# Kernel tuning notes

Hardware: AMD Instinct MI355X
Metric: run time of the kernel (lower is better)

The kernel has to match this reference:

```python
import jax, jax.numpy as jnp
import numpy as np

H = 8          # n_heads
THRESH = 0.5   # edge pruning threshold
LN_EPS = 1e-5


def setup_inputs() -> dict:
    key = jax.random.key(0)
    ks = jax.random.split(key, 24)
    B, S, D = 8, 128, 256
    N = S + 1
    hd = D // H

    def lin(k, fan_in, fan_out, gain=1.0):
        # xavier_uniform-ish init, stored as [in, out] (y = x @ W + b)
        lim = gain * np.sqrt(6.0 / (fan_in + fan_out))
        return jax.random.uniform(k, (fan_in, fan_out), jnp.float32, -lim, lim)

    g = 1.0 / np.sqrt(2.0)
    return {
        "desc": jax.random.normal(ks[0], (B, S, D), jnp.float32),
        "nv": jax.random.normal(ks[1], (B, N, D), jnp.float32),
        "W_gt": lin(ks[2], D, D), "b_gt": jnp.zeros((D,), jnp.float32),
        "topo_bias": jnp.zeros((1,), jnp.float32),
        "W_q": lin(ks[3], D, D, g), "b_q": jnp.zeros((D,), jnp.float32),
        "W_k": lin(ks[4], D, D, g), "b_k": jnp.zeros((D,), jnp.float32),
        "W_v": lin(ks[5], D, D, g), "b_v": jnp.zeros((D,), jnp.float32),
        "W_e1": lin(ks[6], 2 * D, D), "b_e1": jnp.zeros((D,), jnp.float32),
        "ln_g": jnp.ones((D,), jnp.float32), "ln_b": jnp.zeros((D,), jnp.float32),
        "W_e2": lin(ks[7], D, D), "b_e2": jnp.zeros((D,), jnp.float32),
        "w_attn": lin(ks[8], 3 * hd, 1, g)[:, 0], "b_attn": jnp.zeros((), jnp.float32),
        "W_o": lin(ks[9], D, D, g), "b_o": jnp.zeros((D,), jnp.float32),
    }


def _forward(desc, nv, W_gt, b_gt, topo_bias, W_q, b_q, W_k, b_k, W_v, b_v,
             W_e1, b_e1, ln_g, ln_b, W_e2, b_e2, w_attn, b_attn, W_o, b_o):
    B, N, D = nv.shape
    S = N - 1
    hd = D // H

    # 1. global topology
    d = desc @ W_gt + b_gt                                   # [B,S,D]
    dn = d / jnp.linalg.norm(d, axis=-1, keepdims=True)
    global_top = jax.nn.sigmoid(jnp.einsum('bid,bjd->bij', dn, dn) + topo_bias[0])

    # 2. sample-wise similarity
    var = nv[:, 1:, :]
    vn = var / jnp.linalg.norm(var, axis=-1, keepdims=True)
    sample_sim = jnp.einsum('bid,bjd->bij', vn, vn)
    adj_mat = global_top * sample_sim

    # 3. remove self-connection, squash
    diag_mask = 1.0 - jnp.eye(S, dtype=adj_mat.dtype)
    adj = jax.nn.sigmoid(adj_mat * diag_mask)

    # 4. straight-through edge pruning (frozen=False path)
    hard = (adj > THRESH).astype(adj.dtype)
    adj = hard - jax.lax.stop_gradient(adj) + adj

    # 5. edge attributes: Linear(concat(d_i,d_j)) decomposed into two matmuls
    a = d @ W_e1[:D]                                          # node_i part [B,S,D]
    b_ = d @ W_e1[D:]                                         # node_j part [B,S,D]
    pre = jnp.zeros((B, N, N, D), dtype=d.dtype)
    pre = pre.at[:, 1:, 1:].set(a[:, :, None, :] + b_[:, None, :, :])
    cls = a + b_                                              # concat(d_j,d_j) rows
    pre = pre.at[:, 0, 1:].set(cls).at[:, 1:, 0].set(cls)
    pre = pre + b_e1                                          # (0,0) entry = bias only (zeros input)
    mu = pre.mean(-1, keepdims=True)
    vr = ((pre - mu) ** 2).mean(-1, keepdims=True)
    e = jax.nn.relu((pre - mu) * jax.lax.rsqrt(vr + LN_EPS) * ln_g + ln_b)
    e = e @ W_e2 + b_e2                                       # [B,N,N,D]
    e = e.reshape(B, N, N, H, hd).transpose(0, 3, 1, 2, 4)    # [B,H,N,N,hd]

    # padded adjacency: CLS row attends to all vars, col 0 masked
    na = jnp.zeros((B, N, N), dtype=adj.dtype)
    na = na.at[:, 1:, 1:].set(adj).at[:, 0, 1:].set(1.0)
    e = e * na[:, None, :, :, None]

    # 6. additive attention: attn_proj(concat(q,k,e)) decomposed
    q = (nv @ W_q + b_q).reshape(B, N, H, hd).transpose(0, 2, 1, 3)
    k = (nv @ W_k + b_k).reshape(B, N, H, hd).transpose(0, 2, 1, 3)
    v = (nv @ W_v + b_v).reshape(B, N, H, hd).transpose(0, 2, 1, 3)
    wq, wk, we = w_attn[:hd], w_attn[hd:2 * hd], w_attn[2 * hd:]
    scores = (jnp.einsum('bhid,d->bhi', q, wq)[:, :, :, None]
              + jnp.einsum('bhjd,d->bhj', k, wk)[:, :, None, :]
              + jnp.einsum('bhijd,d->bhij', e, we) + b_attn)
    scores = scores + (na[:, None, :, :] == 0).astype(scores.dtype) * -1e9
    attn = jax.nn.softmax(scores, axis=-1)                    # dropout = identity (eval)

    ctx = jnp.einsum('bhij,bhjd->bhid', attn, v)
    out = ctx.transpose(0, 2, 1, 3).reshape(B, N, D) @ W_o + b_o
    return out, attn


def reference(desc, nv, W_gt, b_gt, topo_bias, W_q, b_q, W_k, b_k, W_v, b_v,
              W_e1, b_e1, ln_g, ln_b, W_e2, b_e2, w_attn, b_attn, W_o, b_o):
    return _forward(desc, nv, W_gt, b_gt, topo_bias, W_q, b_q, W_k, b_k, W_v, b_v,
                    W_e1, b_e1, ln_g, ln_b, W_e2, b_e2, w_attn, b_attn, W_o, b_o)
```

## Files before the change

kernel.cpp:

```cpp
#include <hip/hip_runtime.h>
#include <math.h>

#define BB 8
#define SS 128
#define NN 129
#define DD 256
#define HH 8
#define LN_EPS 1e-5f

#define OFF_A    0
#define OFF_BPT  262144
#define OFF_CPT  524288
#define OFF_VART 786432
#define OFF_V    1048576
#define OFF_SQ   1312768
#define OFF_SK   1321024
#define OFF_MA   1329280
#define OFF_QA   1330304
#define OFF_MB   1331328
#define OFF_QB   1332352
#define OFF_MC   1333376
#define OFF_QC   1334400
#define OFF_U    1335424
#define OFF_UB   1337472

__global__ __launch_bounds__(256) void ka2(
    const float* __restrict__ desc, const float* __restrict__ nv,
    const float* __restrict__ W_gt, const float* __restrict__ b_gt,
    const float* __restrict__ W_e1, const float* __restrict__ b_e1,
    const float* __restrict__ W_q, const float* __restrict__ b_q,
    const float* __restrict__ W_k, const float* __restrict__ b_k,
    const float* __restrict__ W_v, const float* __restrict__ b_v,
    const float* __restrict__ W_e2, const float* __restrict__ b_e2,
    const float* __restrict__ w_attn,
    float* __restrict__ a, float* __restrict__ bp_t, float* __restrict__ cp_t,
    float* __restrict__ var_t, float* __restrict__ v,
    float* __restrict__ sq, float* __restrict__ sk,
    float* __restrict__ ma, float* __restrict__ qa, float* __restrict__ mb,
    float* __restrict__ qb, float* __restrict__ mc, float* __restrict__ qc,
    float* __restrict__ U, float* __restrict__ ubias) {
    const int bx = blockIdx.x, t = threadIdx.x;
    __shared__ __attribute__((aligned(16))) float rowbuf[DD][4];
    __shared__ __attribute__((aligned(16))) float drow[DD][4];
    __shared__ float part[24][4];

    if (bx < 256) {
        const int b = bx >> 5, s0 = (bx & 31) * 4;
        for (int e = t; e < 4 * DD; e += 256) {
            int r = e >> 8, k = e & 255;
            rowbuf[k][r] = desc[(size_t)(b * SS + s0 + r) * DD + k];
        }
        __syncthreads();
        const int c = t;
        {
            float dv[4] = {0.f, 0.f, 0.f, 0.f};
#pragma unroll 8
            for (int k = 0; k < DD; k++) {
                float w = W_gt[k * DD + c];
                float4 d4 = *(const float4*)&rowbuf[k][0];
                dv[0] = fmaf(d4.x, w, dv[0]); dv[1] = fmaf(d4.y, w, dv[1]);
                dv[2] = fmaf(d4.z, w, dv[2]); dv[3] = fmaf(d4.w, w, dv[3]);
            }
            float bg = b_gt[c];
            float4 st; st.x = dv[0] + bg; st.y = dv[1] + bg; st.z = dv[2] + bg; st.w = dv[3] + bg;
            *(float4*)&drow[c][0] = st;
        }
        __syncthreads();
        float av[4] = {0.f, 0.f, 0.f, 0.f}, bv[4] = {0.f, 0.f, 0.f, 0.f};
#pragma unroll 4
        for (int k = 0; k < DD; k++) {
            float wa = W_e1[k * DD + c];
            float wb = W_e1[(DD + k) * DD + c];
            float4 d4 = *(const float4*)&drow[k][0];
            av[0] = fmaf(d4.x, wa, av[0]); av[1] = fmaf(d4.y, wa, av[1]);
            av[2] = fmaf(d4.z, wa, av[2]); av[3] = fmaf(d4.w, wa, av[3]);
            bv[0] = fmaf(d4.x, wb, bv[0]); bv[1] = fmaf(d4.y, wb, bv[1]);
            bv[2] = fmaf(d4.z, wb, bv[2]); bv[3] = fmaf(d4.w, wb, bv[3]);
        }
        float be1 = b_e1[c];
        float cv[4];
#pragma unroll
        for (int r = 0; r < 4; r++) { bv[r] += be1; cv[r] = av[r] + bv[r]; }
#pragma unroll
        for (int r = 0; r < 4; r++) a[(size_t)(b * SS + s0 + r) * DD + c] = av[r];
        float4 f4;
        f4.x = bv[0]; f4.y = bv[1]; f4.z = bv[2]; f4.w = bv[3];
        *(float4*)(bp_t + (size_t)(b * DD + c) * SS + s0) = f4;
        f4.x = cv[0]; f4.y = cv[1]; f4.z = cv[2]; f4.w = cv[3];
        *(float4*)(cp_t + (size_t)(b * DD + c) * SS + s0) = f4;
        float nvv[4];
#pragma unroll
        for (int r = 0; r < 4; r++) nvv[r] = nv[(size_t)(b * NN + 1 + s0 + r) * DD + c];
        f4.x = nvv[0]; f4.y = nvv[1]; f4.z = nvv[2]; f4.w = nvv[3];
        *(float4*)(var_t + (size_t)(b * DD + c) * SS + s0) = f4;
        float vals[24];
#pragma unroll
        for (int r = 0; r < 4; r++) {
            vals[r * 6 + 0] = av[r]; vals[r * 6 + 1] = av[r] * av[r];
            vals[r * 6 + 2] = bv[r]; vals[r * 6 + 3] = bv[r] * bv[r];
            vals[r * 6 + 4] = cv[r]; vals[r * 6 + 5] = cv[r] * cv[r];
        }
        int lane = t & 63, wid = t >> 6;
#pragma unroll
        for (int vv = 0; vv < 24; vv++) {
            float x = vals[vv];
            for (int o = 32; o; o >>= 1) x += __shfl_xor(x, o, 64);
            if (lane == 0) part[vv][wid] = x;
        }
        __syncthreads();
        if (t < 24) {
            float ssum = (part[t][0] + part[t][1]) + (part[t][2] + part[t][3]);
            int st = t % 6;
            int row = b * SS + s0 + t / 6;
            float m = ssum * (1.f / DD);
            float* dstp = (st == 0) ? ma : (st == 1) ? qa : (st == 2) ? mb
                         : (st == 3) ? qb : (st == 4) ? mc : qc;
            dstp[row] = m;
        }
    } else if (bx < 520) {
        const int idx = bx - 256;
        const int b = idx / 33, n0 = (idx % 33) * 4;
        for (int e = t; e < 4 * DD; e += 256) {
            int r = e >> 8, k = e & 255;
            int n = n0 + r; if (n >= NN) n = NN - 1;
            rowbuf[k][r] = nv[(size_t)(b * NN + n) * DD + k];
        }
        __syncthreads();
        const int c = t;
        float qv[4] = {0.f, 0.f, 0.f, 0.f}, kv[4] = {0.f, 0.f, 0.f, 0.f},
              vv[4] = {0.f, 0.f, 0.f, 0.f};
#pragma unroll 4
        for (int k = 0; k < DD; k++) {
            float wq = W_q[k * DD + c], wk = W_k[k * DD + c], wvv = W_v[k * DD + c];
            float4 r4 = *(const float4*)&rowbuf[k][0];
            qv[0] = fmaf(r4.x, wq, qv[0]); qv[1] = fmaf(r4.y, wq, qv[1]);
            qv[2] = fmaf(r4.z, wq, qv[2]); qv[3] = fmaf(r4.w, wq, qv[3]);
            kv[0] = fmaf(r4.x, wk, kv[0]); kv[1] = fmaf(r4.y, wk, kv[1]);
            kv[2] = fmaf(r4.z, wk, kv[2]); kv[3] = fmaf(r4.w, wk, kv[3]);
            vv[0] = fmaf(r4.x, wvv, vv[0]); vv[1] = fmaf(r4.y, wvv, vv[1]);
            vv[2] = fmaf(r4.z, wvv, vv[2]); vv[3] = fmaf(r4.w, wvv, vv[3]);
        }
        float bq = b_q[c], bk = b_k[c], bvb = b_v[c];
        float waq = w_attn[c & 31];
        float wak = w_attn[32 + (c & 31)];
        int h = c >> 5;
#pragma unroll
        for (int r = 0; r < 4; r++) {
            int n = n0 + r;
            if (n < NN) v[(size_t)(b * NN + n) * DD + c] = vv[r] + bvb;
            float xq = (qv[r] + bq) * waq, xk = (kv[r] + bk) * wak;
#pragma unroll
            for (int o = 16; o; o >>= 1) { xq += __shfl_xor(xq, o); xk += __shfl_xor(xk, o); }
            if ((c & 31) == 0 && n < NN) {
                sq[(size_t)(b * HH + h) * NN + n] = xq;
                sk[(size_t)(b * HH + h) * NN + n] = xk;
            }
        }
    } else {
        const int ri = bx - 520;
        const int c = t;
        const float wec = w_attn[64 + (c & 31)];
#pragma unroll
        for (int rr = 0; rr < 4; rr++) {
            int r = ri * 4 + rr;
            float x = W_e2[(size_t)r * DD + c] * wec;
#pragma unroll
            for (int o = 16; o; o >>= 1) x += __shfl_xor(x, o);
            if ((c & 31) == 0) U[r * HH + (c >> 5)] = x;
        }
        if (ri == 0) {
            float x = b_e2[c] * wec;
#pragma unroll
            for (int o = 16; o; o >>= 1) x += __shfl_xor(x, o);
            if ((c & 31) == 0) ubias[c >> 5] = x;
        }
    }
}

__global__ __launch_bounds__(256) void kb2(
    const float* __restrict__ a, const float* __restrict__ bp_t, const float* __restrict__ cp_t,
    const float* __restrict__ var_t, const float* __restrict__ nv,
    const float* __restrict__ ma, const float* __restrict__ qa,
    const float* __restrict__ mb, const float* __restrict__ qb,
    const float* __restrict__ mc, const float* __restrict__ qc,
    const float* __restrict__ sq, const float* __restrict__ sk,
    const float* __restrict__ ln_g, const float* __restrict__ ln_b,
    const float* __restrict__ U, const float* __restrict__ ubias,
    const float* __restrict__ b_attn,
    float* __restrict__ attn) {
    const int i = blockIdx.x, b = blockIdx.y;
    const int t = threadIdx.x, jq = t & 31, dg = t >> 5;
    __shared__ float Arow[DD];
    __shared__ float Vrow[DD];
    __shared__ float2 lnsm[DD];
    __shared__ __attribute__((aligned(16))) float4 Usm[DD][2];
    __shared__ __attribute__((aligned(16))) float rsm[SS], nmm[SS], mkm[SS], pnm[SS];
    __shared__ float sqb[HH], ubm[HH];
    __shared__ float sc[HH][132];
    __shared__ __attribute__((aligned(16))) float red[8][HH * SS];

    Arow[t] = (i >= 1) ? a[((size_t)b * SS + i - 1) * DD + t] : 0.f;
    Vrow[t] = nv[((size_t)b * NN + i) * DD + t];
    { float2 g; g.x = ln_g[t]; g.y = ln_b[t]; lnsm[t] = g; }
    Usm[t][0] = *(const float4*)&U[t * HH];
    Usm[t][1] = *(const float4*)&U[t * HH + 4];
    if (t < HH) {
        sqb[t] = sq[(size_t)b * HH * NN + t * NN + i] + b_attn[0];
        ubm[t] = ubias[t];
    }
    __syncthreads();

    if (i >= 1) {
        float cr[4] = {0.f, 0.f, 0.f, 0.f}, dv[4] = {0.f, 0.f, 0.f, 0.f};
        const float* bc = bp_t + ((size_t)b * DD + dg * 32) * SS + 4 * jq;
        const float* vc = var_t + ((size_t)b * DD + dg * 32) * SS + 4 * jq;
#pragma unroll 8
        for (int dd = 0; dd < 32; dd++) {
            float4 b4 = *(const float4*)(bc + (size_t)dd * SS);
            float4 v4 = *(const float4*)(vc + (size_t)dd * SS);
            float A = Arow[dg * 32 + dd], V = Vrow[dg * 32 + dd];
            cr[0] = fmaf(A, b4.x, cr[0]); cr[1] = fmaf(A, b4.y, cr[1]);
            cr[2] = fmaf(A, b4.z, cr[2]); cr[3] = fmaf(A, b4.w, cr[3]);
            dv[0] = fmaf(V, v4.x, dv[0]); dv[1] = fmaf(V, v4.y, dv[1]);
            dv[2] = fmaf(V, v4.z, dv[2]); dv[3] = fmaf(V, v4.w, dv[3]);
        }
        float4 s0; s0.x = cr[0]; s0.y = cr[1]; s0.z = cr[2]; s0.w = cr[3];
        float4 s1; s1.x = dv[0]; s1.y = dv[1]; s1.z = dv[2]; s1.w = dv[3];
        *(float4*)&red[dg][4 * jq] = s0;
        *(float4*)&red[dg][SS + 4 * jq] = s1;
    }
    __syncthreads();
    if (t < SS) {
        const int j = t;
        float rs, nm, mk, pen;
        if (i == 0) {
            float mu = mc[b * SS + j], q2 = qc[b * SS + j];
            rs = rsqrtf(q2 - mu * mu + LN_EPS); nm = -mu * rs; mk = 1.f; pen = 0.f;
        } else {
            float cr = 0.f, dv = 0.f;
#pragma unroll
            for (int g = 0; g < 8; g++) { cr += red[g][j]; dv += red[g][SS + j]; }
            float muA = ma[b * SS + i - 1], qA = qa[b * SS + i - 1];
            float muB = mb[b * SS + j], qB = qb[b * SS + j];
            float mu = muA + muB;
            float var = qA + qB + 2.f * cr * (1.f / DD) - mu * mu;
            rs = rsqrtf(var + LN_EPS); nm = -mu * rs;
            mk = ((i - 1) != j && dv > 0.f) ? 1.f : 0.f;
            pen = (mk == 0.f) ? -1e9f : 0.f;
        }
        rsm[j] = rs; nmm[j] = nm; mkm[j] = mk; pnm[j] = pen;
    }
    __syncthreads();

    float acc[4][HH];
#pragma unroll
    for (int jj = 0; jj < 4; jj++)
#pragma unroll
        for (int h = 0; h < HH; h++) acc[jj][h] = 0.f;
    {
        const float* Bp = ((i == 0) ? cp_t : bp_t) + ((size_t)b * DD + dg * 32) * SS + 4 * jq;
        float4 rs4 = *(const float4*)&rsm[4 * jq];
        float4 nm4 = *(const float4*)&nmm[4 * jq];
        float rsv[4] = {rs4.x, rs4.y, rs4.z, rs4.w};
        float nmv[4] = {nm4.x, nm4.y, nm4.z, nm4.w};
#pragma unroll 4
        for (int dd = 0; dd < 32; dd++) {
            const int d2 = dg * 32 + dd;
            float4 b4 = *(const float4*)(Bp + (size_t)dd * SS);
            float A = Arow[d2];
            float2 gb = lnsm[d2];
            float4 u0 = Usm[d2][0], u1 = Usm[d2][1];
            float bj[4] = {b4.x, b4.y, b4.z, b4.w};
#pragma unroll
            for (int jj = 0; jj < 4; jj++) {
                float y = fmaf(A + bj[jj], rsv[jj], nmv[jj]);
                y = fmaf(y, gb.x, gb.y);
                float rr = fmaxf(y, 0.f);
                acc[jj][0] = fmaf(rr, u0.x, acc[jj][0]);
                acc[jj][1] = fmaf(rr, u0.y, acc[jj][1]);
                acc[jj][2] = fmaf(rr, u0.z, acc[jj][2]);
                acc[jj][3] = fmaf(rr, u0.w, acc[jj][3]);
                acc[jj][4] = fmaf(rr, u1.x, acc[jj][4]);
                acc[jj][5] = fmaf(rr, u1.y, acc[jj][5]);
                acc[jj][6] = fmaf(rr, u1.z, acc[jj][6]);
                acc[jj][7] = fmaf(rr, u1.w, acc[jj][7]);
            }
        }
    }
#pragma unroll
    for (int h = 0; h < HH; h++) {
        float4 w4;
        w4.x = acc[0][h]; w4.y = acc[1][h]; w4.z = acc[2][h]; w4.w = acc[3][h];
        *(float4*)&red[dg][h * SS + 4 * jq] = w4;
    }
    __syncthreads();
    {
        const int j = t >> 1, hb = (t & 1) * 4;
#pragma unroll
        for (int hh = 0; hh < 4; hh++) {
            int h = hb + hh;
            float s = 0.f;
#pragma unroll
            for (int g = 0; g < 8; g++) s += red[g][h * SS + j];
            float skv = sk[(size_t)b * HH * NN + h * NN + 1 + j];
            sc[h][1 + j] = sqb[h] + skv + (s + ubm[h]) * mkm[j] + pnm[j];
        }
    }
    if (t < HH) sc[t][0] = sqb[t] + sk[(size_t)b * HH * NN + t * NN] - 1e9f;
    __syncthreads();

    {
        const int h = t >> 5, l = t & 31;
        float m = -INFINITY;
        for (int jj = l; jj < NN; jj += 32) m = fmaxf(m, sc[h][jj]);
#pragma unroll
        for (int o = 16; o; o >>= 1) m = fmaxf(m, __shfl_xor(m, o));
        float s = 0.f;
        for (int jj = l; jj < NN; jj += 32) { float e = __expf(sc[h][jj] - m); sc[h][jj] = e; s += e; }
#pragma unroll
        for (int o = 16; o; o >>= 1) s += __shfl_xor(s, o);
        float inv = 1.f / s;
        float* arow = attn + (((size_t)b * HH + h) * NN + i) * NN;
        for (int jj = l; jj < NN; jj += 32) arow[jj] = sc[h][jj] * inv;
    }
}

__global__ __launch_bounds__(256) void kc2(
    const float* __restrict__ attn, const float* __restrict__ v,
    const float* __restrict__ W_o, const float* __restrict__ b_o,
    float* __restrict__ out) {
    const int b = blockIdx.y, i0 = blockIdx.x * 2;
    const int t = threadIdx.x;
    __shared__ float ar[2][HH * 132];
    __shared__ __attribute__((aligned(8))) float csm[DD][2];
    for (int e = t; e < 2 * HH * NN; e += 256) {
        int il = e / (HH * NN), r = e - il * (HH * NN);
        int h = r / NN, j = r - h * NN;
        int i = i0 + il; if (i >= NN) i = NN - 1;
        ar[il][h * 132 + j] = attn[(((size_t)b * HH + h) * NN + i) * NN + j];
    }
    __syncthreads();
    {
        const int d = t, h = d >> 5;
        float c0 = 0.f, c1 = 0.f;
        const float* vp = v + (size_t)b * NN * DD + d;
#pragma unroll 4
        for (int j = 0; j < NN; j++) {
            float vv = vp[(size_t)j * DD];
            c0 = fmaf(ar[0][h * 132 + j], vv, c0);
            c1 = fmaf(ar[1][h * 132 + j], vv, c1);
        }
        csm[d][0] = c0; csm[d][1] = c1;
    }
    __syncthreads();
    {
        const int c = t;
        float o0 = 0.f, o1 = 0.f;
#pragma unroll 8
        for (int k = 0; k < DD; k++) {
            float w = W_o[(size_t)k * DD + c];
            float2 cv = *(const float2*)&csm[k][0];
            o0 = fmaf(cv.x, w, o0); o1 = fmaf(cv.y, w, o1);
        }
        float bo = b_o[c];
        out[((size_t)b * NN + i0) * DD + c] = o0 + bo;
        if (i0 + 1 < NN) out[((size_t)b * NN + i0 + 1) * DD + c] = o1 + bo;
    }
}

extern "C" void kernel_launch(void* const* d_in, const int* in_sizes, int n_in,
                              void* d_out, int out_size, void* d_ws, size_t ws_size,
                              hipStream_t stream) {
    const float* desc   = (const float*)d_in[0];
    const float* nv     = (const float*)d_in[1];
    const float* W_gt   = (const float*)d_in[2];
    const float* b_gt   = (const float*)d_in[3];
    const float* W_q    = (const float*)d_in[5];
    const float* b_q    = (const float*)d_in[6];
    const float* W_k    = (const float*)d_in[7];
    const float* b_k    = (const float*)d_in[8];
    const float* W_v    = (const float*)d_in[9];
    const float* b_v    = (const float*)d_in[10];
    const float* W_e1   = (const float*)d_in[11];
    const float* b_e1   = (const float*)d_in[12];
    const float* ln_g   = (const float*)d_in[13];
    const float* ln_b   = (const float*)d_in[14];
    const float* W_e2   = (const float*)d_in[15];
    const float* b_e2   = (const float*)d_in[16];
    const float* w_attn = (const float*)d_in[17];
    const float* b_attn = (const float*)d_in[18];
    const float* W_o    = (const float*)d_in[19];
    const float* b_o    = (const float*)d_in[20];

    float* ws   = (float*)d_ws;
    float* a    = ws + OFF_A;
    float* bp_t = ws + OFF_BPT;
    float* cp_t = ws + OFF_CPT;
    float* vart = ws + OFF_VART;
    float* v    = ws + OFF_V;
    float* sq   = ws + OFF_SQ;
    float* sk   = ws + OFF_SK;
    float* ma   = ws + OFF_MA;
    float* qa   = ws + OFF_QA;
    float* mb   = ws + OFF_MB;
    float* qb   = ws + OFF_QB;
    float* mc   = ws + OFF_MC;
    float* qc   = ws + OFF_QC;
    float* U    = ws + OFF_U;
    float* ub   = ws + OFF_UB;

    float* out  = (float*)d_out;
    float* attn = (float*)d_out + (size_t)BB * NN * DD;

    ka2<<<dim3(584), dim3(256), 0, stream>>>(
        desc, nv, W_gt, b_gt, W_e1, b_e1, W_q, b_q, W_k, b_k, W_v, b_v,
        W_e2, b_e2, w_attn,
        a, bp_t, cp_t, vart, v, sq, sk, ma, qa, mb, qb, mc, qc, U, ub);
    kb2<<<dim3(NN, BB), dim3(256), 0, stream>>>(
        a, bp_t, cp_t, vart, nv, ma, qa, mb, qb, mc, qc, sq, sk,
        ln_g, ln_b, U, ub, b_attn, attn);
    kc2<<<dim3((NN + 1) / 2, BB), dim3(256), 0, stream>>>(attn, v, W_o, b_o, out);
}
```

Before: 191.2 us.

## Precompute Gram matrices in separate kernel and widen row tiles across kernels

```diff
diff --git a/kernel.cpp b/kernel.cpp
--- a/kernel.cpp
+++ b/kernel.cpp
@@ -23,8 +23,10 @@
 #define OFF_QC   1334400
 #define OFF_U    1335424
 #define OFF_UB   1337472
-
-__global__ __launch_bounds__(256) void ka2(
+#define OFF_G    1337600
+#define OFF_VV   1468672
+
+__global__ __launch_bounds__(256) void ka3(
     const float* __restrict__ desc, const float* __restrict__ nv,
     const float* __restrict__ W_gt, const float* __restrict__ b_gt,
     const float* __restrict__ W_e1, const float* __restrict__ b_e1,
@@ -40,75 +42,93 @@
     float* __restrict__ qb, float* __restrict__ mc, float* __restrict__ qc,
     float* __restrict__ U, float* __restrict__ ubias) {
     const int bx = blockIdx.x, t = threadIdx.x;
-    __shared__ __attribute__((aligned(16))) float rowbuf[DD][4];
-    __shared__ __attribute__((aligned(16))) float drow[DD][4];
-    __shared__ float part[24][4];
-
-    if (bx < 256) {
-        const int b = bx >> 5, s0 = (bx & 31) * 4;
-        for (int e = t; e < 4 * DD; e += 256) {
+    __shared__ __attribute__((aligned(16))) float rowbuf[DD][8];
+    __shared__ __attribute__((aligned(16))) float drow[DD][8];
+    __shared__ float part[48][4];
+
+    if (bx < 128) {
+        const int b = bx >> 4, s0 = (bx & 15) * 8;
+        for (int e = t; e < 8 * DD; e += 256) {
             int r = e >> 8, k = e & 255;
             rowbuf[k][r] = desc[(size_t)(b * SS + s0 + r) * DD + k];
         }
         __syncthreads();
         const int c = t;
         {
-            float dv[4] = {0.f, 0.f, 0.f, 0.f};
+            float dv[8] = {0.f, 0.f, 0.f, 0.f, 0.f, 0.f, 0.f, 0.f};
 #pragma unroll 8
             for (int k = 0; k < DD; k++) {
                 float w = W_gt[k * DD + c];
-                float4 d4 = *(const float4*)&rowbuf[k][0];
-                dv[0] = fmaf(d4.x, w, dv[0]); dv[1] = fmaf(d4.y, w, dv[1]);
-                dv[2] = fmaf(d4.z, w, dv[2]); dv[3] = fmaf(d4.w, w, dv[3]);
+                float4 d0 = *(const float4*)&rowbuf[k][0];
+                float4 d1 = *(const float4*)&rowbuf[k][4];
+                dv[0] = fmaf(d0.x, w, dv[0]); dv[1] = fmaf(d0.y, w, dv[1]);
+                dv[2] = fmaf(d0.z, w, dv[2]); dv[3] = fmaf(d0.w, w, dv[3]);
+                dv[4] = fmaf(d1.x, w, dv[4]); dv[5] = fmaf(d1.y, w, dv[5]);
+                dv[6] = fmaf(d1.z, w, dv[6]); dv[7] = fmaf(d1.w, w, dv[7]);
             }
             float bg = b_gt[c];
-            float4 st; st.x = dv[0] + bg; st.y = dv[1] + bg; st.z = dv[2] + bg; st.w = dv[3] + bg;
-            *(float4*)&drow[c][0] = st;
+            float4 s0v, s1v;
+            s0v.x = dv[0] + bg; s0v.y = dv[1] + bg; s0v.z = dv[2] + bg; s0v.w = dv[3] + bg;
+            s1v.x = dv[4] + bg; s1v.y = dv[5] + bg; s1v.z = dv[6] + bg; s1v.w = dv[7] + bg;
+            *(float4*)&drow[c][0] = s0v;
+            *(float4*)&drow[c][4] = s1v;
         }
         __syncthreads();
-        float av[4] = {0.f, 0.f, 0.f, 0.f}, bv[4] = {0.f, 0.f, 0.f, 0.f};
+        float av[8] = {0.f, 0.f, 0.f, 0.f, 0.f, 0.f, 0.f, 0.f};
+        float bv[8] = {0.f, 0.f, 0.f, 0.f, 0.f, 0.f, 0.f, 0.f};
 #pragma unroll 4
         for (int k = 0; k < DD; k++) {
             float wa = W_e1[k * DD + c];
             float wb = W_e1[(DD + k) * DD + c];
-            float4 d4 = *(const float4*)&drow[k][0];
-            av[0] = fmaf(d4.x, wa, av[0]); av[1] = fmaf(d4.y, wa, av[1]);
-            av[2] = fmaf(d4.z, wa, av[2]); av[3] = fmaf(d4.w, wa, av[3]);
-            bv[0] = fmaf(d4.x, wb, bv[0]); bv[1] = fmaf(d4.y, wb, bv[1]);
-            bv[2] = fmaf(d4.z, wb, bv[2]); bv[3] = fmaf(d4.w, wb, bv[3]);
+            float4 d0 = *(const float4*)&drow[k][0];
+            float4 d1 = *(const float4*)&drow[k][4];
+            av[0] = fmaf(d0.x, wa, av[0]); av[1] = fmaf(d0.y, wa, av[1]);
+            av[2] = fmaf(d0.z, wa, av[2]); av[3] = fmaf(d0.w, wa, av[3]);
+            av[4] = fmaf(d1.x, wa, av[4]); av[5] = fmaf(d1.y, wa, av[5]);
+            av[6] = fmaf(d1.z, wa, av[6]); av[7] = fmaf(d1.w, wa, av[7]);
+            bv[0] = fmaf(d0.x, wb, bv[0]); bv[1] = fmaf(d0.y, wb, bv[1]);
+            bv[2] = fmaf(d0.z, wb, bv[2]); bv[3] = fmaf(d0.w, wb, bv[3]);
+            bv[4] = fmaf(d1.x, wb, bv[4]); bv[5] = fmaf(d1.y, wb, bv[5]);
+            bv[6] = fmaf(d1.z, wb, bv[6]); bv[7] = fmaf(d1.w, wb, bv[7]);
         }
         float be1 = b_e1[c];
-        float cv[4];
-#pragma unroll
-        for (int r = 0; r < 4; r++) { bv[r] += be1; cv[r] = av[r] + bv[r]; }
-#pragma unroll
-        for (int r = 0; r < 4; r++) a[(size_t)(b * SS + s0 + r) * DD + c] = av[r];
+        float cv[8];
+#pragma unroll
+        for (int r = 0; r < 8; r++) { bv[r] += be1; cv[r] = av[r] + bv[r]; }
+#pragma unroll
+        for (int r = 0; r < 8; r++) a[(size_t)(b * SS + s0 + r) * DD + c] = av[r];
         float4 f4;
         f4.x = bv[0]; f4.y = bv[1]; f4.z = bv[2]; f4.w = bv[3];
         *(float4*)(bp_t + (size_t)(b * DD + c) * SS + s0) = f4;
+        f4.x = bv[4]; f4.y = bv[5]; f4.z = bv[6]; f4.w = bv[7];
+        *(float4*)(bp_t + (size_t)(b * DD + c) * SS + s0 + 4) = f4;
         f4.x = cv[0]; f4.y = cv[1]; f4.z = cv[2]; f4.w = cv[3];
         *(float4*)(cp_t + (size_t)(b * DD + c) * SS + s0) = f4;
-        float nvv[4];
-#pragma unroll
-        for (int r = 0; r < 4; r++) nvv[r] = nv[(size_t)(b * NN + 1 + s0 + r) * DD + c];
+        f4.x = cv[4]; f4.y = cv[5]; f4.z = cv[6]; f4.w = cv[7];
+        *(float4*)(cp_t + (size_t)(b * DD + c) * SS + s0 + 4) = f4;
+        float nvv[8];
+#pragma unroll
+        for (int r = 0; r < 8; r++) nvv[r] = nv[(size_t)(b * NN + 1 + s0 + r) * DD + c];
         f4.x = nvv[0]; f4.y = nvv[1]; f4.z = nvv[2]; f4.w = nvv[3];
         *(float4*)(var_t + (size_t)(b * DD + c) * SS + s0) = f4;
-        float vals[24];
-#pragma unroll
-        for (int r = 0; r < 4; r++) {
+        f4.x = nvv[4]; f4.y = nvv[5]; f4.z = nvv[6]; f4.w = nvv[7];
+        *(float4*)(var_t + (size_t)(b * DD + c) * SS + s0 + 4) = f4;
+        float vals[48];
+#pragma unroll
+        for (int r = 0; r < 8; r++) {
             vals[r * 6 + 0] = av[r]; vals[r * 6 + 1] = av[r] * av[r];
             vals[r * 6 + 2] = bv[r]; vals[r * 6 + 3] = bv[r] * bv[r];
             vals[r * 6 + 4] = cv[r]; vals[r * 6 + 5] = cv[r] * cv[r];
         }
         int lane = t & 63, wid = t >> 6;
 #pragma unroll
-        for (int vv = 0; vv < 24; vv++) {
+        for (int vv = 0; vv < 48; vv++) {
             float x = vals[vv];
             for (int o = 32; o; o >>= 1) x += __shfl_xor(x, o, 64);
             if (lane == 0) part[vv][wid] = x;
         }
         __syncthreads();
-        if (t < 24) {
+        if (t < 48) {
             float ssum = (part[t][0] + part[t][1]) + (part[t][2] + part[t][3]);
             int st = t % 6;
             int row = b * SS + s0 + t / 6;
@@ -117,35 +137,43 @@
                          : (st == 3) ? qb : (st == 4) ? mc : qc;
             dstp[row] = m;
         }
-    } else if (bx < 520) {
-        const int idx = bx - 256;
-        const int b = idx / 33, n0 = (idx % 33) * 4;
-        for (int e = t; e < 4 * DD; e += 256) {
+    } else if (bx < 264) {
+        const int idx = bx - 128;
+        const int b = idx / 17, n0 = (idx % 17) * 8;
+        for (int e = t; e < 8 * DD; e += 256) {
             int r = e >> 8, k = e & 255;
             int n = n0 + r; if (n >= NN) n = NN - 1;
             rowbuf[k][r] = nv[(size_t)(b * NN + n) * DD + k];
         }
         __syncthreads();
         const int c = t;
-        float qv[4] = {0.f, 0.f, 0.f, 0.f}, kv[4] = {0.f, 0.f, 0.f, 0.f},
-              vv[4] = {0.f, 0.f, 0.f, 0.f};
+        float qv[8] = {0.f, 0.f, 0.f, 0.f, 0.f, 0.f, 0.f, 0.f};
+        float kv[8] = {0.f, 0.f, 0.f, 0.f, 0.f, 0.f, 0.f, 0.f};
+        float vv[8] = {0.f, 0.f, 0.f, 0.f, 0.f, 0.f, 0.f, 0.f};
 #pragma unroll 4
         for (int k = 0; k < DD; k++) {
             float wq = W_q[k * DD + c], wk = W_k[k * DD + c], wvv = W_v[k * DD + c];
-            float4 r4 = *(const float4*)&rowbuf[k][0];
-            qv[0] = fmaf(r4.x, wq, qv[0]); qv[1] = fmaf(r4.y, wq, qv[1]);
-            qv[2] = fmaf(r4.z, wq, qv[2]); qv[3] = fmaf(r4.w, wq, qv[3]);
-            kv[0] = fmaf(r4.x, wk, kv[0]); kv[1] = fmaf(r4.y, wk, kv[1]);
-            kv[2] = fmaf(r4.z, wk, kv[2]); kv[3] = fmaf(r4.w, wk, kv[3]);
-            vv[0] = fmaf(r4.x, wvv, vv[0]); vv[1] = fmaf(r4.y, wvv, vv[1]);
-            vv[2] = fmaf(r4.z, wvv, vv[2]); vv[3] = fmaf(r4.w, wvv, vv[3]);
+            float4 r0 = *(const float4*)&rowbuf[k][0];
+            float4 r1 = *(const float4*)&rowbuf[k][4];
+            qv[0] = fmaf(r0.x, wq, qv[0]); qv[1] = fmaf(r0.y, wq, qv[1]);
+            qv[2] = fmaf(r0.z, wq, qv[2]); qv[3] = fmaf(r0.w, wq, qv[3]);
+            qv[4] = fmaf(r1.x, wq, qv[4]); qv[5] = fmaf(r1.y, wq, qv[5]);
+            qv[6] = fmaf(r1.z, wq, qv[6]); qv[7] = fmaf(r1.w, wq, qv[7]);
+            kv[0] = fmaf(r0.x, wk, kv[0]); kv[1] = fmaf(r0.y, wk, kv[1]);
+            kv[2] = fmaf(r0.z, wk, kv[2]); kv[3] = fmaf(r0.w, wk, kv[3]);
+            kv[4] = fmaf(r1.x, wk, kv[4]); kv[5] = fmaf(r1.y, wk, kv[5]);
+            kv[6] = fmaf(r1.z, wk, kv[6]); kv[7] = fmaf(r1.w, wk, kv[7]);
+            vv[0] = fmaf(r0.x, wvv, vv[0]); vv[1] = fmaf(r0.y, wvv, vv[1]);
+            vv[2] = fmaf(r0.z, wvv, vv[2]); vv[3] = fmaf(r0.w, wvv, vv[3]);
+            vv[4] = fmaf(r1.x, wvv, vv[4]); vv[5] = fmaf(r1.y, wvv, vv[5]);
+            vv[6] = fmaf(r1.z, wvv, vv[6]); vv[7] = fmaf(r1.w, wvv, vv[7]);
         }
         float bq = b_q[c], bk = b_k[c], bvb = b_v[c];
         float waq = w_attn[c & 31];
         float wak = w_attn[32 + (c & 31)];
         int h = c >> 5;
 #pragma unroll
-        for (int r = 0; r < 4; r++) {
+        for (int r = 0; r < 8; r++) {
             int n = n0 + r;
             if (n < NN) v[(size_t)(b * NN + n) * DD + c] = vv[r] + bvb;
             float xq = (qv[r] + bq) * waq, xk = (kv[r] + bk) * wak;
@@ -157,7 +185,7 @@
             }
         }
     } else {
-        const int ri = bx - 520;
+        const int ri = bx - 264;
         const int c = t;
         const float wec = w_attn[64 + (c & 31)];
 #pragma unroll
@@ -177,194 +205,240 @@
     }
 }
 
-__global__ __launch_bounds__(256) void kb2(
+__global__ __launch_bounds__(256) void kgram(
+    const float* __restrict__ a, const float* __restrict__ bp_t,
+    const float* __restrict__ nv, const float* __restrict__ var_t,
+    float* __restrict__ G, float* __restrict__ VV) {
+    const int bx = blockIdx.x, t = threadIdx.x;
+    const bool isG = bx < 128;
+    const int idx = isG ? bx : bx - 128;
+    const int b = idx >> 4, tl = idx & 15;
+    const int i0 = (tl >> 1) * 16, j0 = (tl & 1) * 64;
+    const float* Asrc = isG ? (a + ((size_t)b * SS + i0) * DD)
+                            : (nv + ((size_t)b * NN + 1 + i0) * DD);
+    const float* Bt = (isG ? bp_t : var_t) + (size_t)b * DD * SS;
+    float* C = (isG ? G : VV) + (size_t)b * SS * SS;
+    __shared__ __attribute__((aligned(16))) float Al[16][DD];
+    for (int e = t; e < 16 * DD / 4; e += 256) {
+        int r = e >> 6, c4 = e & 63;
+        *(float4*)&Al[r][c4 * 4] = *(const float4*)&Asrc[(size_t)r * DD + c4 * 4];
+    }
+    __syncthreads();
+    const int dg = t & 3, jl = t >> 2;
+    float acc[16] = {0.f, 0.f, 0.f, 0.f, 0.f, 0.f, 0.f, 0.f,
+                     0.f, 0.f, 0.f, 0.f, 0.f, 0.f, 0.f, 0.f};
+    const float* bp = Bt + (size_t)(dg * 64) * SS + j0 + jl;
+#pragma unroll 4
+    for (int dd = 0; dd < 64; dd++) {
+        float bvv = bp[(size_t)dd * SS];
+        int d = dg * 64 + dd;
+#pragma unroll
+        for (int i = 0; i < 16; i++) acc[i] = fmaf(Al[i][d], bvv, acc[i]);
+    }
+#pragma unroll
+    for (int i = 0; i < 16; i++) {
+        acc[i] += __shfl_xor(acc[i], 1);
+        acc[i] += __shfl_xor(acc[i], 2);
+    }
+    if (dg == 0) {
+#pragma unroll
+        for (int i = 0; i < 16; i++) C[(size_t)(i0 + i) * SS + j0 + jl] = acc[i];
+    }
+}
+
+__global__ __launch_bounds__(256) void kb3(
     const float* __restrict__ a, const float* __restrict__ bp_t, const float* __restrict__ cp_t,
-    const float* __restrict__ var_t, const float* __restrict__ nv,
     const float* __restrict__ ma, const float* __restrict__ qa,
     const float* __restrict__ mb, const float* __restrict__ qb,
     const float* __restrict__ mc, const float* __restrict__ qc,
+    const float* __restrict__ G, const float* __restrict__ VV,
     const float* __restrict__ sq, const float* __restrict__ sk,
     const float* __restrict__ ln_g, const float* __restrict__ ln_b,
     const float* __restrict__ U, const float* __restrict__ ubias,
     const float* __restrict__ b_attn,
     float* __restrict__ attn) {
-    const int i = blockIdx.x, b = blockIdx.y;
-    const int t = threadIdx.x, jq = t & 31, dg = t >> 5;
-    __shared__ float Arow[DD];
-    __shared__ float Vrow[DD];
-    __shared__ float2 lnsm[DD];
+    const int it = blockIdx.x, b = blockIdx.y;
+    const int i0 = it * 2;
+    const int t = threadIdx.x;
+    const int dg = t >> 6, jl = t & 63;
+    __shared__ float Arow[2][DD];
+    __shared__ __attribute__((aligned(8))) float2 lnsm[DD];
     __shared__ __attribute__((aligned(16))) float4 Usm[DD][2];
-    __shared__ __attribute__((aligned(16))) float rsm[SS], nmm[SS], mkm[SS], pnm[SS];
-    __shared__ float sqb[HH], ubm[HH];
-    __shared__ float sc[HH][132];
-    __shared__ __attribute__((aligned(16))) float red[8][HH * SS];
-
-    Arow[t] = (i >= 1) ? a[((size_t)b * SS + i - 1) * DD + t] : 0.f;
-    Vrow[t] = nv[((size_t)b * NN + i) * DD + t];
-    { float2 g; g.x = ln_g[t]; g.y = ln_b[t]; lnsm[t] = g; }
-    Usm[t][0] = *(const float4*)&U[t * HH];
-    Usm[t][1] = *(const float4*)&U[t * HH + 4];
-    if (t < HH) {
-        sqb[t] = sq[(size_t)b * HH * NN + t * NN + i] + b_attn[0];
-        ubm[t] = ubias[t];
-    }
-    __syncthreads();
-
-    if (i >= 1) {
-        float cr[4] = {0.f, 0.f, 0.f, 0.f}, dv[4] = {0.f, 0.f, 0.f, 0.f};
-        const float* bc = bp_t + ((size_t)b * DD + dg * 32) * SS + 4 * jq;
-        const float* vc = var_t + ((size_t)b * DD + dg * 32) * SS + 4 * jq;
-#pragma unroll 8
-        for (int dd = 0; dd < 32; dd++) {
-            float4 b4 = *(const float4*)(bc + (size_t)dd * SS);
-            float4 v4 = *(const float4*)(vc + (size_t)dd * SS);
-            float A = Arow[dg * 32 + dd], V = Vrow[dg * 32 + dd];
-            cr[0] = fmaf(A, b4.x, cr[0]); cr[1] = fmaf(A, b4.y, cr[1]);
-            cr[2] = fmaf(A, b4.z, cr[2]); cr[3] = fmaf(A, b4.w, cr[3]);
-            dv[0] = fmaf(V, v4.x, dv[0]); dv[1] = fmaf(V, v4.y, dv[1]);
-            dv[2] = fmaf(V, v4.z, dv[2]); dv[3] = fmaf(V, v4.w, dv[3]);
-        }
-        float4 s0; s0.x = cr[0]; s0.y = cr[1]; s0.z = cr[2]; s0.w = cr[3];
-        float4 s1; s1.x = dv[0]; s1.y = dv[1]; s1.z = dv[2]; s1.w = dv[3];
-        *(float4*)&red[dg][4 * jq] = s0;
-        *(float4*)&red[dg][SS + 4 * jq] = s1;
+    __shared__ __attribute__((aligned(8))) float rsm[2][SS], nmm[2][SS], mkm[2][SS], pnm[2][SS];
+    __shared__ float skm[HH * NN];
+    __shared__ float sqb[2][HH], ubm[HH];
+    __shared__ float sc[2][HH][NN + 3];
+    __shared__ __attribute__((aligned(8))) float red[4][2][HH][SS];
+
+    {
+        int ic0 = i0, ic1 = (i0 + 1 < NN) ? i0 + 1 : NN - 1;
+        Arow[0][t] = (ic0 >= 1) ? a[((size_t)b * SS + ic0 - 1) * DD + t] : 0.f;
+        Arow[1][t] = (ic1 >= 1) ? a[((size_t)b * SS + ic1 - 1) * DD + t] : 0.f;
+        float2 g; g.x = ln_g[t]; g.y = ln_b[t]; lnsm[t] = g;
+        Usm[t][0] = *(const float4*)&U[t * HH];
+        Usm[t][1] = *(const float4*)&U[t * HH + 4];
+        for (int e = t; e < HH * NN; e += 256) skm[e] = sk[(size_t)b * HH * NN + e];
+        if (t < 16) {
+            int il = t >> 3, h = t & 7;
+            int i = i0 + il; if (i > NN - 1) i = NN - 1;
+            sqb[il][h] = sq[(size_t)b * HH * NN + h * NN + i] + b_attn[0];
+        }
+        if (t < HH) ubm[t] = ubias[t];
     }
     __syncthreads();
     if (t < SS) {
         const int j = t;
-        float rs, nm, mk, pen;
-        if (i == 0) {
-            float mu = mc[b * SS + j], q2 = qc[b * SS + j];
-            rs = rsqrtf(q2 - mu * mu + LN_EPS); nm = -mu * rs; mk = 1.f; pen = 0.f;
-        } else {
-            float cr = 0.f, dv = 0.f;
-#pragma unroll
-            for (int g = 0; g < 8; g++) { cr += red[g][j]; dv += red[g][SS + j]; }
-            float muA = ma[b * SS + i - 1], qA = qa[b * SS + i - 1];
-            float muB = mb[b * SS + j], qB = qb[b * SS + j];
-            float mu = muA + muB;
-            float var = qA + qB + 2.f * cr * (1.f / DD) - mu * mu;
-            rs = rsqrtf(var + LN_EPS); nm = -mu * rs;
-            mk = ((i - 1) != j && dv > 0.f) ? 1.f : 0.f;
-            pen = (mk == 0.f) ? -1e9f : 0.f;
-        }
-        rsm[j] = rs; nmm[j] = nm; mkm[j] = mk; pnm[j] = pen;
-    }
-    __syncthreads();
-
-    float acc[4][HH];
-#pragma unroll
-    for (int jj = 0; jj < 4; jj++)
-#pragma unroll
-        for (int h = 0; h < HH; h++) acc[jj][h] = 0.f;
+#pragma unroll
+        for (int il = 0; il < 2; il++) {
+            int i = i0 + il; if (i > NN - 1) i = NN - 1;
+            float rs, nm, mk, pen;
+            if (i == 0) {
+                float mu = mc[b * SS + j], q2 = qc[b * SS + j];
+                rs = rsqrtf(q2 - mu * mu + LN_EPS); nm = -mu * rs; mk = 1.f; pen = 0.f;
+            } else {
+                float cr = G[((size_t)b * SS + i - 1) * SS + j];
+                float dv = VV[((size_t)b * SS + i - 1) * SS + j];
+                float muA = ma[b * SS + i - 1], qA = qa[b * SS + i - 1];
+                float muB = mb[b * SS + j], qB = qb[b * SS + j];
+                float mu = muA + muB;
+                float var = qA + qB + 2.f * cr * (1.f / DD) - mu * mu;
+                rs = rsqrtf(var + LN_EPS); nm = -mu * rs;
+                mk = ((i - 1) != j && dv > 0.f) ? 1.f : 0.f;
+                pen = (mk == 0.f) ? -1e9f : 0.f;
+            }
+            rsm[il][j] = rs; nmm[il][j] = nm; mkm[il][j] = mk; pnm[il][j] = pen;
+        }
+    }
+    __syncthreads();
+    float acc[2][HH][2];
+#pragma unroll
+    for (int il = 0; il < 2; il++)
+#pragma unroll
+        for (int h = 0; h < HH; h++) { acc[il][h][0] = 0.f; acc[il][h][1] = 0.f; }
     {
-        const float* Bp = ((i == 0) ? cp_t : bp_t) + ((size_t)b * DD + dg * 32) * SS + 4 * jq;
-        float4 rs4 = *(const float4*)&rsm[4 * jq];
-        float4 nm4 = *(const float4*)&nmm[4 * jq];
-        float rsv[4] = {rs4.x, rs4.y, rs4.z, rs4.w};
-        float nmv[4] = {nm4.x, nm4.y, nm4.z, nm4.w};
+        const float* B0 = ((i0 == 0) ? cp_t : bp_t) + ((size_t)b * DD + dg * 64) * SS + 2 * jl;
+        const float* B1 = bp_t + ((size_t)b * DD + dg * 64) * SS + 2 * jl;
+        float2 r0 = *(const float2*)&rsm[0][2 * jl];
+        float2 n0 = *(const float2*)&nmm[0][2 * jl];
+        float2 r1 = *(const float2*)&rsm[1][2 * jl];
+        float2 n1 = *(const float2*)&nmm[1][2 * jl];
 #pragma unroll 4
-        for (int dd = 0; dd < 32; dd++) {
-            const int d2 = dg * 32 + dd;
-            float4 b4 = *(const float4*)(Bp + (size_t)dd * SS);
-            float A = Arow[d2];
-            float2 gb = lnsm[d2];
-            float4 u0 = Usm[d2][0], u1 = Usm[d2][1];
-            float bj[4] = {b4.x, b4.y, b4.z, b4.w};
-#pragma unroll
-            for (int jj = 0; jj < 4; jj++) {
-                float y = fmaf(A + bj[jj], rsv[jj], nmv[jj]);
-                y = fmaf(y, gb.x, gb.y);
-                float rr = fmaxf(y, 0.f);
-                acc[jj][0] = fmaf(rr, u0.x, acc[jj][0]);
-                acc[jj][1] = fmaf(rr, u0.y, acc[jj][1]);
-                acc[jj][2] = fmaf(rr, u0.z, acc[jj][2]);
-                acc[jj][3] = fmaf(rr, u0.w, acc[jj][3]);
-                acc[jj][4] = fmaf(rr, u1.x, acc[jj][4]);
-                acc[jj][5] = fmaf(rr, u1.y, acc[jj][5]);
-                acc[jj][6] = fmaf(rr, u1.z, acc[jj][6]);
-                acc[jj][7] = fmaf(rr, u1.w, acc[jj][7]);
+        for (int dd = 0; dd < 64; dd++) {
+            const int d = dg * 64 + dd;
+            float2 bA = *(const float2*)(B0 + (size_t)dd * SS);
+            float2 bB = *(const float2*)(B1 + (size_t)dd * SS);
+            float A0 = Arow[0][d], A1 = Arow[1][d];
+            float2 gb = lnsm[d];
+            float4 u0 = Usm[d][0], u1 = Usm[d][1];
+            {
+                float y0 = fmaf(A0 + bA.x, r0.x, n0.x); y0 = fmaf(y0, gb.x, gb.y);
+                float y1 = fmaf(A0 + bA.y, r0.y, n0.y); y1 = fmaf(y1, gb.x, gb.y);
+                float e0 = fmaxf(y0, 0.f), e1 = fmaxf(y1, 0.f);
+                acc[0][0][0] = fmaf(e0, u0.x, acc[0][0][0]); acc[0][0][1] = fmaf(e1, u0.x, acc[0][0][1]);
+                acc[0][1][0] = fmaf(e0, u0.y, acc[0][1][0]); acc[0][1][1] = fmaf(e1, u0.y, acc[0][1][1]);
+                acc[0][2][0] = fmaf(e0, u0.z, acc[0][2][0]); acc[0][2][1] = fmaf(e1, u0.z, acc[0][2][1]);
+                acc[0][3][0] = fmaf(e0, u0.w, acc[0][3][0]); acc[0][3][1] = fmaf(e1, u0.w, acc[0][3][1]);
+                acc[0][4][0] = fmaf(e0, u1.x, acc[0][4][0]); acc[0][4][1] = fmaf(e1, u1.x, acc[0][4][1]);
+                acc[0][5][0] = fmaf(e0, u1.y, acc[0][5][0]); acc[0][5][1] = fmaf(e1, u1.y, acc[0][5][1]);
+                acc[0][6][0] = fmaf(e0, u1.z, acc[0][6][0]); acc[0][6][1] = fmaf(e1, u1.z, acc[0][6][1]);
+                acc[0][7][0] = fmaf(e0, u1.w, acc[0][7][0]); acc[0][7][1] = fmaf(e1, u1.w, acc[0][7][1]);
             }
-        }
-    }
-#pragma unroll
-    for (int h = 0; h < HH; h++) {
-        float4 w4;
-        w4.x = acc[0][h]; w4.y = acc[1][h]; w4.z = acc[2][h]; w4.w = acc[3][h];
-        *(float4*)&red[dg][h * SS + 4 * jq] = w4;
-    }
+            {
+                float y0 = fmaf(A1 + bB.x, r1.x, n1.x); y0 = fmaf(y0, gb.x, gb.y);
+                float y1 = fmaf(A1 + bB.y, r1.y, n1.y); y1 = fmaf(y1, gb.x, gb.y);
+                float e0 = fmaxf(y0, 0.f), e1 = fmaxf(y1, 0.f);
+                acc[1][0][0] = fmaf(e0, u0.x, acc[1][0][0]); acc[1][0][1] = fmaf(e1, u0.x, acc[1][0][1]);
+                acc[1][1][0] = fmaf(e0, u0.y, acc[1][1][0]); acc[1][1][1] = fmaf(e1, u0.y, acc[1][1][1]);
+                acc[1][2][0] = fmaf(e0, u0.z, acc[1][2][0]); acc[1][2][1] = fmaf(e1, u0.z, acc[1][2][1]);
+                acc[1][3][0] = fmaf(e0, u0.w, acc[1][3][0]); acc[1][3][1] = fmaf(e1, u0.w, acc[1][3][1]);
+                acc[1][4][0] = fmaf(e0, u1.x, acc[1][4][0]); acc[1][4][1] = fmaf(e1, u1.x, acc[1][4][1]);
+                acc[1][5][0] = fmaf(e0, u1.y, acc[1][5][0]); acc[1][5][1] = fmaf(e1, u1.y, acc[1][5][1]);
+                acc[1][6][0] = fmaf(e0, u1.z, acc[1][6][0]); acc[1][6][1] = fmaf(e1, u1.z, acc[1][6][1]);
+                acc[1][7][0] = fmaf(e0, u1.w, acc[1][7][0]); acc[1][7][1] = fmaf(e1, u1.w, acc[1][7][1]);
+            }
+        }
+    }
+#pragma unroll
+    for (int il = 0; il < 2; il++)
+#pragma unroll
+        for (int h = 0; h < HH; h++) {
+            float2 w; w.x = acc[il][h][0]; w.y = acc[il][h][1];
+            *(float2*)&red[dg][il][h][2 * jl] = w;
+        }
+    __syncthreads();
+    for (int e = t; e < 2 * HH * SS; e += 256) {
+        int il = e >> 10, h = (e >> 7) & 7, j = e & 127;
+        float s = (red[0][il][h][j] + red[1][il][h][j]) + (red[2][il][h][j] + red[3][il][h][j]);
+        sc[il][h][1 + j] = sqb[il][h] + skm[h * NN + 1 + j] + (s + ubm[h]) * mkm[il][j] + pnm[il][j];
+    }
+    if (t < 16) { int il = t >> 3, h = t & 7; sc[il][h][0] = sqb[il][h] + skm[h * NN] - 1e9f; }
     __syncthreads();
     {
-        const int j = t >> 1, hb = (t & 1) * 4;
-#pragma unroll
-        for (int hh = 0; hh < 4; hh++) {
-            int h = hb + hh;
-            float s = 0.f;
-#pragma unroll
-            for (int g = 0; g < 8; g++) s += red[g][h * SS + j];
-            float skv = sk[(size_t)b * HH * NN + h * NN + 1 + j];
-            sc[h][1 + j] = sqb[h] + skv + (s + ubm[h]) * mkm[j] + pnm[j];
-        }
-    }
-    if (t < HH) sc[t][0] = sqb[t] + sk[(size_t)b * HH * NN + t * NN] - 1e9f;
-    __syncthreads();
-
-    {
-        const int h = t >> 5, l = t & 31;
+        const int row = t >> 4, l = t & 15;
+        const int il = row >> 3, h = row & 7;
+        const int i = i0 + il;
         float m = -INFINITY;
-        for (int jj = l; jj < NN; jj += 32) m = fmaxf(m, sc[h][jj]);
-#pragma unroll
-        for (int o = 16; o; o >>= 1) m = fmaxf(m, __shfl_xor(m, o));
+        for (int j = l; j < NN; j += 16) m = fmaxf(m, sc[il][h][j]);
+#pragma unroll
+        for (int o = 8; o; o >>= 1) m = fmaxf(m, __shfl_xor(m, o, 16));
         float s = 0.f;
-        for (int jj = l; jj < NN; jj += 32) { float e = __expf(sc[h][jj] - m); sc[h][jj] = e; s += e; }
-#pragma unroll
-        for (int o = 16; o; o >>= 1) s += __shfl_xor(s, o);
+        for (int j = l; j < NN; j += 16) { float e = __expf(sc[il][h][j] - m); sc[il][h][j] = e; s += e; }
+#pragma unroll
+        for (int o = 8; o; o >>= 1) s += __shfl_xor(s, o, 16);
         float inv = 1.f / s;
-        float* arow = attn + (((size_t)b * HH + h) * NN + i) * NN;
-        for (int jj = l; jj < NN; jj += 32) arow[jj] = sc[h][jj] * inv;
+        if (i < NN) {
+            float* arow = attn + (((size_t)b * HH + h) * NN + i) * NN;
+            for (int j = l; j < NN; j += 16) arow[j] = sc[il][h][j] * inv;
+        }
     }
 }
 
-__global__ __launch_bounds__(256) void kc2(
+__global__ __launch_bounds__(256) void kc3(
     const float* __restrict__ attn, const float* __restrict__ v,
     const float* __restrict__ W_o, const float* __restrict__ b_o,
     float* __restrict__ out) {
-    const int b = blockIdx.y, i0 = blockIdx.x * 2;
+    const int b = blockIdx.y, i0 = blockIdx.x * 4;
     const int t = threadIdx.x;
-    __shared__ float ar[2][HH * 132];
-    __shared__ __attribute__((aligned(8))) float csm[DD][2];
-    for (int e = t; e < 2 * HH * NN; e += 256) {
-        int il = e / (HH * NN), r = e - il * (HH * NN);
-        int h = r / NN, j = r - h * NN;
+    __shared__ float ar[4][HH * 132];
+    __shared__ float csmT[4][DD];
+    for (int e = t; e < 4 * HH * NN; e += 256) {
+        int il = e / (HH * NN), rem = e - il * (HH * NN);
+        int h = rem / NN, j = rem - h * NN;
         int i = i0 + il; if (i >= NN) i = NN - 1;
         ar[il][h * 132 + j] = attn[(((size_t)b * HH + h) * NN + i) * NN + j];
     }
     __syncthreads();
     {
         const int d = t, h = d >> 5;
-        float c0 = 0.f, c1 = 0.f;
+        float c0 = 0.f, c1 = 0.f, c2 = 0.f, c3 = 0.f;
         const float* vp = v + (size_t)b * NN * DD + d;
 #pragma unroll 4
         for (int j = 0; j < NN; j++) {
             float vv = vp[(size_t)j * DD];
             c0 = fmaf(ar[0][h * 132 + j], vv, c0);
             c1 = fmaf(ar[1][h * 132 + j], vv, c1);
-        }
-        csm[d][0] = c0; csm[d][1] = c1;
+            c2 = fmaf(ar[2][h * 132 + j], vv, c2);
+            c3 = fmaf(ar[3][h * 132 + j], vv, c3);
+        }
+        csmT[0][d] = c0; csmT[1][d] = c1; csmT[2][d] = c2; csmT[3][d] = c3;
     }
     __syncthreads();
     {
         const int c = t;
-        float o0 = 0.f, o1 = 0.f;
+        float o0 = 0.f, o1 = 0.f, o2 = 0.f, o3 = 0.f;
 #pragma unroll 8
         for (int k = 0; k < DD; k++) {
             float w = W_o[(size_t)k * DD + c];
-            float2 cv = *(const float2*)&csm[k][0];
-            o0 = fmaf(cv.x, w, o0); o1 = fmaf(cv.y, w, o1);
+            o0 = fmaf(csmT[0][k], w, o0); o1 = fmaf(csmT[1][k], w, o1);
+            o2 = fmaf(csmT[2][k], w, o2); o3 = fmaf(csmT[3][k], w, o3);
         }
         float bo = b_o[c];
-        out[((size_t)b * NN + i0) * DD + c] = o0 + bo;
-        if (i0 + 1 < NN) out[((size_t)b * NN + i0 + 1) * DD + c] = o1 + bo;
+        float o[4] = {o0, o1, o2, o3};
+#pragma unroll
+        for (int il = 0; il < 4; il++) {
+            int i = i0 + il;
+            if (i < NN) out[((size_t)b * NN + i) * DD + c] = o[il] + bo;
+        }
     }
 }
 
@@ -408,16 +482,19 @@
     float* qc   = ws + OFF_QC;
     float* U    = ws + OFF_U;
     float* ub   = ws + OFF_UB;
+    float* G    = ws + OFF_G;
+    float* VV   = ws + OFF_VV;
 
     float* out  = (float*)d_out;
     float* attn = (float*)d_out + (size_t)BB * NN * DD;
 
-    ka2<<<dim3(584), dim3(256), 0, stream>>>(
+    ka3<<<dim3(328), dim3(256), 0, stream>>>(
         desc, nv, W_gt, b_gt, W_e1, b_e1, W_q, b_q, W_k, b_k, W_v, b_v,
         W_e2, b_e2, w_attn,
         a, bp_t, cp_t, vart, v, sq, sk, ma, qa, mb, qb, mc, qc, U, ub);
-    kb2<<<dim3(NN, BB), dim3(256), 0, stream>>>(
-        a, bp_t, cp_t, vart, nv, ma, qa, mb, qb, mc, qc, sq, sk,
+    kgram<<<dim3(256), dim3(256), 0, stream>>>(a, bp_t, nv, vart, G, VV);
+    kb3<<<dim3(65, BB), dim3(256), 0, stream>>>(
+        a, bp_t, cp_t, ma, qa, mb, qb, mc, qc, G, VV, sq, sk,
         ln_g, ln_b, U, ub, b_attn, attn);
-    kc2<<<dim3((NN + 1) / 2, BB), dim3(256), 0, stream>>>(attn, v, W_o, b_o, out);
+    kc3<<<dim3(33, BB), dim3(256), 0, stream>>>(attn, v, W_o, b_o, out);
 }
```

Measured after the change: 211.6 us. 10.6% more time.
